# Kernel tuning notes

Hardware: AMD Instinct MI355X
Metric: run time of the kernel (lower is better)

## Reference

```python
import jax, jax.numpy as jnp
import numpy as np

B, S, D, K = 4, 4096, 1024, 64

def setup_inputs() -> dict:
    key = jax.random.key(0)
    kx, kq, kk, kv, ko = jax.random.split(key, 5)
    scale = 1.0 / np.sqrt(D)
    return {
        "x": jax.random.normal(kx, (B, S, D), dtype=jnp.float32),
        "Wq": jax.random.uniform(kq, (K, D), dtype=jnp.float32, minval=-scale, maxval=scale),
        "Wk": jax.random.uniform(kk, (K, D), dtype=jnp.float32, minval=-scale, maxval=scale),
        "Wv": jax.random.uniform(kv, (K, D), dtype=jnp.float32, minval=-scale, maxval=scale),
        "Wo": jax.random.uniform(ko, (D, K), dtype=jnp.float32, minval=-1.0/np.sqrt(K), maxval=1.0/np.sqrt(K)),
    }

def reference(x, Wq, Wk, Wv, Wo):
    # projections: torch Linear(dim, key_dim, bias=False) -> x @ W.T
    Q = jax.nn.elu(x @ Wq.T) + 1.0          # [B,S,K]
    Kf = jax.nn.elu(x @ Wk.T) + 1.0         # [B,S,K]
    V = x @ Wv.T                             # [B,S,K]
    # causal running KV state via cumsum of outer products: [B,S,K,K]
    KV_sum = jnp.cumsum(Kf[..., :, None] * V[..., None, :], axis=1)
    K_sum = jnp.cumsum(Kf, axis=1)           # [B,S,K]
    num = jnp.einsum('bsk,bskm->bsm', Q, KV_sum)   # [B,S,K]
    den = jnp.einsum('bsk,bsk->bs', Q, K_sum)[..., None]
    out = num / (den + 1e-6)
    return out @ Wo.T                         # [B,S,D]
```

## Files before the change

### kernel.cpp

```cpp
#include <hip/hip_runtime.h>

#define BB 4
#define SS 4096
#define DDIM 1024
#define KDIM 64
#define NCHUNK 64
#define TCHUNK 256
#define MROWS 16384

typedef short short8v __attribute__((ext_vector_type(8)));
typedef float f32x4 __attribute__((ext_vector_type(4)));
#define MFMA16 __builtin_amdgcn_mfma_f32_16x16x32_bf16

__device__ __forceinline__ ushort f2bf(float f) {
    uint u = __float_as_uint(f);
    u += 0x7FFFu + ((u >> 16) & 1u);
    return (ushort)(u >> 16);
}

__global__ __launch_bounds__(256) void k_wconv(
    const float* __restrict__ Wq, const float* __restrict__ Wk,
    const float* __restrict__ Wv, const float* __restrict__ Wo,
    ushort* __restrict__ Whf, ushort* __restrict__ Wof)
{
    const int b = blockIdx.x, t = threadIdx.x;
    const int ks = t >> 7;
    const int l = (t >> 1) & 63;
    const int half = t & 1;
    if (b < 192) {
        const int s = b / 12, cf = b % 12;
        const int grow = cf * 16 + (l & 15);
        const int gcol = s * 64 + ks * 32 + ((l >> 4) & 3) * 8 + half * 4;
        const float* src = (grow < 64) ? (Wq + (size_t)grow * DDIM)
                         : (grow < 128) ? (Wk + (size_t)(grow - 64) * DDIM)
                                        : (Wv + (size_t)(grow - 128) * DDIM);
        float4 v = *(const float4*)&src[gcol];
        ushort* dst = &Whf[(size_t)(((s * 12 + cf) * 2 + ks) * 64 + l) * 8 + half * 4];
        dst[0] = f2bf(v.x); dst[1] = f2bf(v.y); dst[2] = f2bf(v.z); dst[3] = f2bf(v.w);
    } else {
        const int cf = b - 192;
        const int d = cf * 16 + (l & 15);
        const int kc = ks * 32 + ((l >> 4) & 3) * 8 + half * 4;
        float4 v = *(const float4*)&Wo[(size_t)d * KDIM + kc];
        ushort* dst = &Wof[(size_t)((cf * 2 + ks) * 64 + l) * 8 + half * 4];
        dst[0] = f2bf(v.x); dst[1] = f2bf(v.y); dst[2] = f2bf(v.z); dst[3] = f2bf(v.w);
    }
}

#define EBP 216
__global__ __launch_bounds__(512) void k_proj(
    const float* __restrict__ x, const ushort* __restrict__ Whf,
    ushort* __restrict__ Qf, ushort* __restrict__ Kff, ushort* __restrict__ VT,
    float* __restrict__ KVc, float* __restrict__ Ksc)
{
    __shared__ ushort xs[2 * 64 * 512];
    const int t = threadIdx.x;
    const int w = t >> 6, l = t & 63;
    const int rw = w >> 2, cw = w & 3;
    const int g = blockIdx.x;
    const int row0 = g * 64;
    const int lq = l >> 4;

    float4 xr[16];
    auto stageLoad = [&](int h) {
#pragma unroll
        for (int i = 0; i < 8; ++i) {
            const int fidx = i * 512 + t;
            const int r = fidx >> 6;
            const int c = (fidx & 63) * 8;
            const float* p = &x[(size_t)(row0 + r) * DDIM + h * 512 + c];
            xr[i * 2] = *(const float4*)p;
            xr[i * 2 + 1] = *(const float4*)(p + 4);
        }
    };
    auto stageWrite = [&](int buf) {
        ushort* xb = xs + buf * 32768;
#pragma unroll
        for (int i = 0; i < 8; ++i) {
            const int fidx = i * 512 + t;
            const int r = fidx >> 6;
            const int c = (fidx & 63) * 8;
            float4 u0 = xr[i * 2], u1 = xr[i * 2 + 1];
            short8v hh;
            hh[0] = (short)f2bf(u0.x); hh[1] = (short)f2bf(u0.y);
            hh[2] = (short)f2bf(u0.z); hh[3] = (short)f2bf(u0.w);
            hh[4] = (short)f2bf(u1.x); hh[5] = (short)f2bf(u1.y);
            hh[6] = (short)f2bf(u1.z); hh[7] = (short)f2bf(u1.w);
            const int frag = (r >> 4) * 16 + (c >> 5);
            const int slot = ((r & 15) | (((c >> 3) & 3) << 4)) ^ (frag & 7);
            *(short8v*)&xb[(size_t)(frag * 64 + slot) * 8] = hh;
        }
    };

    f32x4 acc[2][3];
#pragma unroll
    for (int r = 0; r < 2; ++r)
#pragma unroll
        for (int c = 0; c < 3; ++c) acc[r][c] = (f32x4){0.f, 0.f, 0.f, 0.f};

    auto loadW = [&](int sg, short8v (&bw)[6]) {
#pragma unroll
        for (int j = 0; j < 6; ++j) {
            const int cf = cw * 3 + (j >> 1);
            const int f = cf * 2 + (j & 1);
            bw[j] = *(const short8v*)&Whf[((size_t)(sg * 24 + f)) * 512 + l * 8];
        }
    };
    auto computeStep = [&](int buf, int sl, short8v (&bw)[6]) {
        const ushort* xb = xs + buf * 32768;
#pragma unroll
        for (int ks = 0; ks < 2; ++ks) {
            const int kkl = sl * 2 + ks;
            const int f0 = (rw * 2) * 16 + kkl;
            const int f1 = (rw * 2 + 1) * 16 + kkl;
            short8v a0 = *(const short8v*)&xb[(size_t)(f0 * 64 + (l ^ (f0 & 7))) * 8];
            short8v a1 = *(const short8v*)&xb[(size_t)(f1 * 64 + (l ^ (f1 & 7))) * 8];
#pragma unroll
            for (int c = 0; c < 3; ++c) {
                acc[0][c] = MFMA16(a0, bw[c * 2 + ks], acc[0][c], 0, 0, 0);
                acc[1][c] = MFMA16(a1, bw[c * 2 + ks], acc[1][c], 0, 0, 0);
            }
        }
    };

    stageLoad(0); stageWrite(0);
    __syncthreads();
    stageLoad(1);
    {
        short8v bwA[6], bwB[6];
        loadW(0, bwA);
        for (int s = 0; s < 8; s += 2) {
            loadW(s + 1, bwB);
            computeStep(0, s, bwA);
            if (s + 2 < 8) loadW(s + 2, bwA);
            computeStep(0, s + 1, bwB);
        }
    }
    stageWrite(1);
    __syncthreads();
    {
        short8v bwA[6], bwB[6];
        loadW(8, bwA);
        for (int s = 0; s < 8; s += 2) {
            loadW(8 + s + 1, bwB);
            computeStep(1, s, bwA);
            if (s + 2 < 8) loadW(8 + s + 2, bwA);
            computeStep(1, s + 1, bwB);
        }
    }

    ushort* eb = xs;
#pragma unroll
    for (int rfi = 0; rfi < 2; ++rfi)
#pragma unroll
        for (int ci = 0; ci < 3; ++ci) {
            const int col = (cw * 3 + ci) * 16 + (l & 15);
#pragma unroll
            for (int q = 0; q < 4; ++q) {
                const int rl = (rw * 2 + rfi) * 16 + lq * 4 + q;
                float v = acc[rfi][ci][q];
                if (col < 128) v = (v > 0.f) ? v + 1.f : __expf(v);
                eb[rl * EBP + col] = f2bf(v);
            }
        }
    __syncthreads();

    {
        const int fj = t >> 6, lam = t & 63;
        const int rh = fj >> 2, rfm = (fj >> 1) & 1, ks = fj & 1;
        const int r = rh * 32 + rfm * 16 + (lam & 15);
        const int c0 = ks * 32 + ((lam >> 4) & 3) * 8;
        short8v q8 = *(const short8v*)&eb[r * EBP + c0];
        short8v k8 = *(const short8v*)&eb[r * EBP + 64 + c0];
        const size_t fo = ((size_t)((g * 2 + rh) * 4 + rfm * 2 + ks)) * 512 + lam * 8;
        *(short8v*)&Qf[fo] = q8;
        *(short8v*)&Kff[fo] = k8;
    }
    {
        const int fj = t >> 6, lam = t & 63;
        const int f = fj >> 1, js = fj & 1;
        const int jb = js * 32 + ((lam >> 4) & 3) * 8;
        const int vcol = 128 + f * 16 + (lam & 15);
        short8v vT;
#pragma unroll
        for (int e = 0; e < 8; ++e) vT[e] = (short)eb[(jb + e) * EBP + vcol];
        *(short8v*)&VT[((size_t)(g * 8 + f * 2 + js)) * 512 + lam * 8] = vT;
    }
    {
        const int kf = w & 3, mh = w >> 2;
        short8v ka[2], vb0[2], vb1[2];
#pragma unroll
        for (int js = 0; js < 2; ++js) {
            const int jb = js * 32 + ((l >> 4) & 3) * 8;
#pragma unroll
            for (int e = 0; e < 8; ++e) {
                const int j = jb + e;
                ka[js][e]  = (short)eb[j * EBP + 64 + kf * 16 + (l & 15)];
                vb0[js][e] = (short)eb[j * EBP + 128 + (mh * 2 + 0) * 16 + (l & 15)];
                vb1[js][e] = (short)eb[j * EBP + 128 + (mh * 2 + 1) * 16 + (l & 15)];
            }
        }
        f32x4 a0 = (f32x4){0.f,0.f,0.f,0.f}, a1 = (f32x4){0.f,0.f,0.f,0.f};
        f32x4 ad = (f32x4){0.f,0.f,0.f,0.f};
        short8v onesf;
#pragma unroll
        for (int e = 0; e < 8; ++e) onesf[e] = ((l & 15) == 0) ? (short)0x3F80 : (short)0;
#pragma unroll
        for (int js = 0; js < 2; ++js) {
            a0 = MFMA16(ka[js], vb0[js], a0, 0, 0, 0);
            a1 = MFMA16(ka[js], vb1[js], a1, 0, 0, 0);
            if (mh == 0) ad = MFMA16(ka[js], onesf, ad, 0, 0, 0);
        }
#pragma unroll
        for (int q = 0; q < 4; ++q) {
            const int k = kf * 16 + lq * 4 + q;
            KVc[(size_t)g * 4096 + k * 64 + (mh * 2 + 0) * 16 + (l & 15)] = a0[q];
            KVc[(size_t)g * 4096 + k * 64 + (mh * 2 + 1) * 16 + (l & 15)] = a1[q];
            if (mh == 0 && (l & 15) == 0) Ksc[(size_t)g * KDIM + k] = ad[q];
        }
    }
}

__global__ void k_scan(const float* __restrict__ KVc, const float* __restrict__ Ksc,
                       float* __restrict__ Sst, float* __restrict__ Kss)
{
    const int b = blockIdx.x / 65;
    const int r = blockIdx.x % 65;
    const int t = threadIdx.x;
    if (r < 64) {
        const int e = r * 64 + t;
        float v[64];
#pragma unroll
        for (int i = 0; i < 64; ++i)
            v[i] = KVc[((size_t)(b * NCHUNK + i)) * 4096 + e];
        float acc = 0.f;
#pragma unroll
        for (int i = 0; i < 64; ++i) {
            Sst[((size_t)(b * NCHUNK + i)) * 4096 + e] = acc;
            acc += v[i];
        }
    } else {
        float v[64];
#pragma unroll
        for (int i = 0; i < 64; ++i)
            v[i] = Ksc[((size_t)(b * NCHUNK + i)) * KDIM + t];
        float acc = 0.f;
#pragma unroll
        for (int i = 0; i < 64; ++i) {
            Kss[((size_t)(b * NCHUNK + i)) * KDIM + t] = acc;
            acc += v[i];
        }
    }
}

__global__ __launch_bounds__(256) void k_intra(
    const ushort* __restrict__ Qf, const ushort* __restrict__ Kff,
    const ushort* __restrict__ VT, const float* __restrict__ Sst,
    const float* __restrict__ Kss, const ushort* __restrict__ Wof,
    float* __restrict__ out)
{
    __shared__ ushort pb[32 * 64];
    __shared__ ushort sT[80 * 64];
    __shared__ float ob[4][16 * 68 + 4];
    const int bx = blockIdx.x, t = threadIdx.x;
    const int g = bx >> 1, rh = bx & 1;
    const int w = t >> 6, l = t & 63;
    const int lq = l >> 4;

    {
        const int k = t >> 2, m0 = (t & 3) * 16;
        const float4* sp = (const float4*)&Sst[(size_t)g * 4096 + k * 64 + m0];
        float4 f0 = sp[0], f1 = sp[1], f2v = sp[2], f3 = sp[3];
        float fv[16] = {f0.x, f0.y, f0.z, f0.w, f1.x, f1.y, f1.z, f1.w,
                        f2v.x, f2v.y, f2v.z, f2v.w, f3.x, f3.y, f3.z, f3.w};
#pragma unroll
        for (int i = 0; i < 16; ++i) {
            const int m = m0 + i;
            sT[m * 64 + (k ^ ((m & 7) << 3))] = f2bf(fv[i]);
        }
        if (t < 64) sT[64 * 64 + t] = f2bf(Kss[(size_t)g * KDIM + t]);
        for (int idx = t; idx < 960; idx += 256) sT[65 * 64 + idx] = 0;
    }

    const int rf = w & 1;
    short8v qa[2];
#pragma unroll
    for (int ks = 0; ks < 2; ++ks)
        qa[ks] = *(const short8v*)&Qf[((size_t)((g * 2 + rh) * 4 + rf * 2 + ks)) * 512 + l * 8];
    {
        const int cfh = w >> 1;
        f32x4 accs[2];
#pragma unroll
        for (int ci = 0; ci < 2; ++ci) accs[ci] = (f32x4){0.f, 0.f, 0.f, 0.f};
#pragma unroll
        for (int ci = 0; ci < 2; ++ci) {
            const int cf = cfh * 2 + ci;
#pragma unroll
            for (int ks = 0; ks < 2; ++ks) {
                short8v kb = *(const short8v*)&Kff[((size_t)((g * 2 + (cf >> 1)) * 4 + (cf & 1) * 2 + ks)) * 512 + l * 8];
                accs[ci] = MFMA16(qa[ks], kb, accs[ci], 0, 0, 0);
            }
        }
#pragma unroll
        for (int ci = 0; ci < 2; ++ci)
#pragma unroll
            for (int q = 0; q < 4; ++q) {
                const int row = rf * 16 + lq * 4 + q;
                const int col = (cfh * 2 + ci) * 16 + (l & 15);
                const float sv = (col <= rh * 32 + row) ? accs[ci][q] : 0.f;
                pb[row * 64 + (col ^ ((row & 7) << 3))] = f2bf(sv);
            }
    }
    __syncthreads();

    const int mg = w >> 1;
    f32x4 an0 = (f32x4){0.f,0.f,0.f,0.f}, an1 = (f32x4){0.f,0.f,0.f,0.f};
    f32x4 ad = (f32x4){0.f,0.f,0.f,0.f};
    short8v onesf;
#pragma unroll
    for (int e = 0; e < 8; ++e) onesf[e] = ((l & 15) == 0) ? (short)0x3F80 : (short)0;
#pragma unroll
    for (int js = 0; js < 2; ++js) {
        const int prow = rf * 16 + (l & 15);
        const int pbase = js * 32 + ((l >> 4) & 3) * 8;
        short8v pa = *(const short8v*)&pb[prow * 64 + (pbase ^ ((prow & 7) << 3))];
        short8v v0 = *(const short8v*)&VT[((size_t)(g * 8 + (mg * 2 + 0) * 2 + js)) * 512 + l * 8];
        short8v v1 = *(const short8v*)&VT[((size_t)(g * 8 + (mg * 2 + 1) * 2 + js)) * 512 + l * 8];
        an0 = MFMA16(pa, v0, an0, 0, 0, 0);
        an1 = MFMA16(pa, v1, an1, 0, 0, 0);
        ad  = MFMA16(pa, onesf, ad, 0, 0, 0);
    }
#pragma unroll
    for (int ks = 0; ks < 2; ++ks) {
        const int base = ks * 32 + ((l >> 4) & 3) * 8;
        const int r0 = (mg * 2 + 0) * 16 + (l & 15);
        const int r1 = (mg * 2 + 1) * 16 + (l & 15);
        const int r4 = 64 + (l & 15);
        short8v s0 = *(const short8v*)&sT[r0 * 64 + (base ^ ((r0 & 7) << 3))];
        short8v s1 = *(const short8v*)&sT[r1 * 64 + (base ^ ((r1 & 7) << 3))];
        short8v s4 = *(const short8v*)&sT[r4 * 64 + (base ^ ((r4 & 7) << 3))];
        an0 = MFMA16(qa[ks], s0, an0, 0, 0, 0);
        an1 = MFMA16(qa[ks], s1, an1, 0, 0, 0);
        ad  = MFMA16(qa[ks], s4, ad, 0, 0, 0);
    }
#pragma unroll
    for (int q = 0; q < 4; ++q) {
        const float den = __shfl(ad[q], (l & 48));
        const float rinv = 1.f / (den + 1e-6f);
        const int row = rf * 16 + lq * 4 + q;
        const int c0 = (mg * 2 + 0) * 16 + (l & 15);
        const int c1 = (mg * 2 + 1) * 16 + (l & 15);
        pb[row * 64 + (c0 ^ ((row & 7) << 3))] = f2bf(an0[q] * rinv);
        pb[row * 64 + (c1 ^ ((row & 7) << 3))] = f2bf(an1[q] * rinv);
    }
    __syncthreads();

    short8v oa[2][2];
#pragma unroll
    for (int rfi = 0; rfi < 2; ++rfi)
#pragma unroll
        for (int ks = 0; ks < 2; ++ks) {
            const int row = rfi * 16 + (l & 15);
            const int base = ks * 32 + ((l >> 4) & 3) * 8;
            oa[rfi][ks] = *(const short8v*)&pb[row * 64 + (base ^ ((row & 7) << 3))];
        }
    float* obw = ob[w];
#pragma unroll
    for (int rr = 0; rr < 4; ++rr) {
        f32x4 acco[2][4];
#pragma unroll
        for (int rfi = 0; rfi < 2; ++rfi)
#pragma unroll
            for (int ci = 0; ci < 4; ++ci) acco[rfi][ci] = (f32x4){0.f, 0.f, 0.f, 0.f};
#pragma unroll
        for (int ci = 0; ci < 4; ++ci) {
            const int cfg = w * 16 + rr * 4 + ci;
#pragma unroll
            for (int ks = 0; ks < 2; ++ks) {
                short8v wb = *(const short8v*)&Wof[((size_t)(cfg * 2 + ks)) * 512 + l * 8];
#pragma unroll
                for (int rfi = 0; rfi < 2; ++rfi)
                    acco[rfi][ci] = MFMA16(oa[rfi][ks], wb, acco[rfi][ci], 0, 0, 0);
            }
        }
#pragma unroll
        for (int rfi = 0; rfi < 2; ++rfi) {
#pragma unroll
            for (int ci = 0; ci < 4; ++ci)
#pragma unroll
                for (int q = 0; q < 4; ++q)
                    obw[(lq * 4 + q) * 68 + ci * 16 + (l & 15)] = acco[rfi][ci][q];
#pragma unroll
            for (int rg = 0; rg < 4; ++rg) {
                const int row = rg * 4 + lq;
                float4 vv = *(const float4*)&obw[row * 68 + (l & 15) * 4];
                *(float4*)&out[((size_t)(g * 64 + rh * 32 + rfi * 16 + row)) * DDIM
                               + w * 256 + rr * 64 + (l & 15) * 4] = vv;
            }
        }
    }
}

extern "C" void kernel_launch(void* const* d_in, const int* in_sizes, int n_in,
                              void* d_out, int out_size, void* d_ws, size_t ws_size,
                              hipStream_t stream)
{
    const float* x  = (const float*)d_in[0];
    const float* Wq = (const float*)d_in[1];
    const float* Wk = (const float*)d_in[2];
    const float* Wv = (const float*)d_in[3];
    const float* Wo = (const float*)d_in[4];
    float* out = (float*)d_out;

    float* ws   = (float*)d_ws;
    float* KVc  = ws;
    float* Sst  = KVc + (size_t)TCHUNK * 4096;
    float* Ksc  = Sst + (size_t)TCHUNK * 4096;
    float* Kss  = Ksc + (size_t)TCHUNK * KDIM;
    ushort* Whf = (ushort*)(Kss + (size_t)TCHUNK * KDIM);
    ushort* Wof = Whf + (size_t)192 * DDIM;
    ushort* Qf  = Wof + (size_t)64 * 1024;
    ushort* Kff = Qf  + (size_t)512 * 4 * 512;
    ushort* VT  = Kff + (size_t)512 * 4 * 512;

    k_wconv<<<dim3(256), dim3(256), 0, stream>>>(Wq, Wk, Wv, Wo, Whf, Wof);
    k_proj<<<dim3(TCHUNK), dim3(512), 0, stream>>>(x, Whf, Qf, Kff, VT, KVc, Ksc);
    k_scan<<<dim3(BB * 65), dim3(64), 0, stream>>>(KVc, Ksc, Sst, Kss);
    k_intra<<<dim3(TCHUNK * 2), dim3(256), 0, stream>>>(Qf, Kff, VT, Sst, Kss, Wof, out);
}
```

Measured before the change: 56.80 us.

## Halve projection tile to 32 rows and split chunk KV sums into new kernel

New measurement: 57.97 us. 1.02x slower.

```diff
diff --git a/kernel.cpp b/kernel.cpp
--- a/kernel.cpp
+++ b/kernel.cpp
@@ -50,53 +50,41 @@
 #define EBP 216
 __global__ __launch_bounds__(512) void k_proj(
     const float* __restrict__ x, const ushort* __restrict__ Whf,
-    ushort* __restrict__ Qf, ushort* __restrict__ Kff, ushort* __restrict__ VT,
-    float* __restrict__ KVc, float* __restrict__ Ksc)
-{
-    __shared__ ushort xs[2 * 64 * 512];
+    ushort* __restrict__ Qf, ushort* __restrict__ Kff,
+    ushort* __restrict__ KfT, ushort* __restrict__ VT)
+{
+    __shared__ ushort xs[64 * 512];
     const int t = threadIdx.x;
     const int w = t >> 6, l = t & 63;
     const int rw = w >> 2, cw = w & 3;
-    const int g = blockIdx.x;
-    const int row0 = g * 64;
+    const int mb = blockIdx.x;
+    const int row0 = mb * 32;
     const int lq = l >> 4;
 
-    float4 xr[16];
-    auto stageLoad = [&](int h) {
+    {
 #pragma unroll
         for (int i = 0; i < 8; ++i) {
-            const int fidx = i * 512 + t;
-            const int r = fidx >> 6;
-            const int c = (fidx & 63) * 8;
-            const float* p = &x[(size_t)(row0 + r) * DDIM + h * 512 + c];
-            xr[i * 2] = *(const float4*)p;
-            xr[i * 2 + 1] = *(const float4*)(p + 4);
-        }
-    };
-    auto stageWrite = [&](int buf) {
-        ushort* xb = xs + buf * 32768;
-#pragma unroll
-        for (int i = 0; i < 8; ++i) {
-            const int fidx = i * 512 + t;
-            const int r = fidx >> 6;
-            const int c = (fidx & 63) * 8;
-            float4 u0 = xr[i * 2], u1 = xr[i * 2 + 1];
+            const int c8 = i * 512 + t;
+            const int r = c8 >> 7;
+            const int col = (c8 & 127) * 8;
+            const float* p = &x[(size_t)(row0 + r) * DDIM + col];
+            float4 u0 = *(const float4*)p;
+            float4 u1 = *(const float4*)(p + 4);
             short8v hh;
             hh[0] = (short)f2bf(u0.x); hh[1] = (short)f2bf(u0.y);
             hh[2] = (short)f2bf(u0.z); hh[3] = (short)f2bf(u0.w);
             hh[4] = (short)f2bf(u1.x); hh[5] = (short)f2bf(u1.y);
             hh[6] = (short)f2bf(u1.z); hh[7] = (short)f2bf(u1.w);
-            const int frag = (r >> 4) * 16 + (c >> 5);
-            const int slot = ((r & 15) | (((c >> 3) & 3) << 4)) ^ (frag & 7);
-            *(short8v*)&xb[(size_t)(frag * 64 + slot) * 8] = hh;
-        }
-    };
-
-    f32x4 acc[2][3];
-#pragma unroll
-    for (int r = 0; r < 2; ++r)
-#pragma unroll
-        for (int c = 0; c < 3; ++c) acc[r][c] = (f32x4){0.f, 0.f, 0.f, 0.f};
+            const int frag = (r >> 4) * 32 + (col >> 5);
+            const int slot = ((r & 15) | (((col >> 3) & 3) << 4)) ^ (frag & 7);
+            *(short8v*)&xs[(size_t)(frag * 64 + slot) * 8] = hh;
+        }
+    }
+    __syncthreads();
+
+    f32x4 acc[3];
+#pragma unroll
+    for (int c = 0; c < 3; ++c) acc[c] = (f32x4){0.f, 0.f, 0.f, 0.f};
 
     auto loadW = [&](int sg, short8v (&bw)[6]) {
 #pragma unroll
@@ -106,117 +94,113 @@
             bw[j] = *(const short8v*)&Whf[((size_t)(sg * 24 + f)) * 512 + l * 8];
         }
     };
-    auto computeStep = [&](int buf, int sl, short8v (&bw)[6]) {
-        const ushort* xb = xs + buf * 32768;
+    auto computeStep = [&](int sl, short8v (&bw)[6]) {
 #pragma unroll
         for (int ks = 0; ks < 2; ++ks) {
-            const int kkl = sl * 2 + ks;
-            const int f0 = (rw * 2) * 16 + kkl;
-            const int f1 = (rw * 2 + 1) * 16 + kkl;
-            short8v a0 = *(const short8v*)&xb[(size_t)(f0 * 64 + (l ^ (f0 & 7))) * 8];
-            short8v a1 = *(const short8v*)&xb[(size_t)(f1 * 64 + (l ^ (f1 & 7))) * 8];
-#pragma unroll
-            for (int c = 0; c < 3; ++c) {
-                acc[0][c] = MFMA16(a0, bw[c * 2 + ks], acc[0][c], 0, 0, 0);
-                acc[1][c] = MFMA16(a1, bw[c * 2 + ks], acc[1][c], 0, 0, 0);
-            }
+            const int f = rw * 32 + sl * 2 + ks;
+            short8v a = *(const short8v*)&xs[(size_t)(f * 64 + (l ^ (f & 7))) * 8];
+#pragma unroll
+            for (int c = 0; c < 3; ++c)
+                acc[c] = MFMA16(a, bw[c * 2 + ks], acc[c], 0, 0, 0);
         }
     };
 
-    stageLoad(0); stageWrite(0);
-    __syncthreads();
-    stageLoad(1);
     {
         short8v bwA[6], bwB[6];
         loadW(0, bwA);
-        for (int s = 0; s < 8; s += 2) {
+        for (int s = 0; s < 16; s += 2) {
             loadW(s + 1, bwB);
-            computeStep(0, s, bwA);
-            if (s + 2 < 8) loadW(s + 2, bwA);
-            computeStep(0, s + 1, bwB);
-        }
-    }
-    stageWrite(1);
+            computeStep(s, bwA);
+            if (s + 2 < 16) loadW(s + 2, bwA);
+            computeStep(s + 1, bwB);
+        }
+    }
+
     __syncthreads();
-    {
-        short8v bwA[6], bwB[6];
-        loadW(8, bwA);
-        for (int s = 0; s < 8; s += 2) {
-            loadW(8 + s + 1, bwB);
-            computeStep(1, s, bwA);
-            if (s + 2 < 8) loadW(8 + s + 2, bwA);
-            computeStep(1, s + 1, bwB);
-        }
-    }
-
     ushort* eb = xs;
 #pragma unroll
-    for (int rfi = 0; rfi < 2; ++rfi)
-#pragma unroll
-        for (int ci = 0; ci < 3; ++ci) {
-            const int col = (cw * 3 + ci) * 16 + (l & 15);
-#pragma unroll
-            for (int q = 0; q < 4; ++q) {
-                const int rl = (rw * 2 + rfi) * 16 + lq * 4 + q;
-                float v = acc[rfi][ci][q];
-                if (col < 128) v = (v > 0.f) ? v + 1.f : __expf(v);
-                eb[rl * EBP + col] = f2bf(v);
-            }
-        }
+    for (int ci = 0; ci < 3; ++ci) {
+        const int col = (cw * 3 + ci) * 16 + (l & 15);
+#pragma unroll
+        for (int q = 0; q < 4; ++q) {
+            const int row = rw * 16 + lq * 4 + q;
+            float v = acc[ci][q];
+            if (col < 128) v = (v > 0.f) ? v + 1.f : __expf(v);
+            eb[row * EBP + col] = f2bf(v);
+        }
+    }
     __syncthreads();
 
     {
-        const int fj = t >> 6, lam = t & 63;
-        const int rh = fj >> 2, rfm = (fj >> 1) & 1, ks = fj & 1;
-        const int r = rh * 32 + rfm * 16 + (lam & 15);
-        const int c0 = ks * 32 + ((lam >> 4) & 3) * 8;
-        short8v q8 = *(const short8v*)&eb[r * EBP + c0];
-        short8v k8 = *(const short8v*)&eb[r * EBP + 64 + c0];
-        const size_t fo = ((size_t)((g * 2 + rh) * 4 + rfm * 2 + ks)) * 512 + lam * 8;
-        *(short8v*)&Qf[fo] = q8;
-        *(short8v*)&Kff[fo] = k8;
-    }
-    {
-        const int fj = t >> 6, lam = t & 63;
-        const int f = fj >> 1, js = fj & 1;
-        const int jb = js * 32 + ((lam >> 4) & 3) * 8;
-        const int vcol = 128 + f * 16 + (lam & 15);
-        short8v vT;
-#pragma unroll
-        for (int e = 0; e < 8; ++e) vT[e] = (short)eb[(jb + e) * EBP + vcol];
-        *(short8v*)&VT[((size_t)(g * 8 + f * 2 + js)) * 512 + lam * 8] = vT;
-    }
-    {
-        const int kf = w & 3, mh = w >> 2;
-        short8v ka[2], vb0[2], vb1[2];
+        const int fj = t >> 6;
+        const int which = fj >> 2, rf = (fj >> 1) & 1, ks = fj & 1;
+        const int r = rf * 16 + (l & 15);
+        const int c0 = ks * 32 + ((l >> 4) & 3) * 8;
+        const size_t fo = ((size_t)(mb * 4 + rf * 2 + ks)) * 512 + l * 8;
+        if (which == 0) {
+            short8v q8 = *(const short8v*)&eb[r * EBP + c0];
+            *(short8v*)&Qf[fo] = q8;
+        } else {
+            short8v k8 = *(const short8v*)&eb[r * EBP + 64 + c0];
+            *(short8v*)&Kff[fo] = k8;
+        }
+    }
+    {
+        const int fj = t >> 6;
+        const int which = fj >> 2, f = fj & 3;
+        const int col = (which ? 128 : 64) + f * 16 + (l & 15);
+        const int jb = ((l >> 4) & 3) * 8;
+        short8v tv;
+#pragma unroll
+        for (int e = 0; e < 8; ++e) tv[e] = (short)eb[(jb + e) * EBP + col];
+        const size_t fo = ((size_t)((mb >> 1) * 8 + f * 2 + (mb & 1))) * 512 + l * 8;
+        if (which == 0) *(short8v*)&KfT[fo] = tv;
+        else            *(short8v*)&VT[fo]  = tv;
+    }
+}
+
+__global__ __launch_bounds__(64) void k_chunksum(
+    const ushort* __restrict__ KfT, const ushort* __restrict__ VT,
+    float* __restrict__ KVc, float* __restrict__ Ksc)
+{
+    const int g = blockIdx.x, l = threadIdx.x;
+    short8v ka[4][2], vb[4][2];
+#pragma unroll
+    for (int f = 0; f < 4; ++f)
 #pragma unroll
         for (int js = 0; js < 2; ++js) {
-            const int jb = js * 32 + ((l >> 4) & 3) * 8;
-#pragma unroll
-            for (int e = 0; e < 8; ++e) {
-                const int j = jb + e;
-                ka[js][e]  = (short)eb[j * EBP + 64 + kf * 16 + (l & 15)];
-                vb0[js][e] = (short)eb[j * EBP + 128 + (mh * 2 + 0) * 16 + (l & 15)];
-                vb1[js][e] = (short)eb[j * EBP + 128 + (mh * 2 + 1) * 16 + (l & 15)];
-            }
-        }
-        f32x4 a0 = (f32x4){0.f,0.f,0.f,0.f}, a1 = (f32x4){0.f,0.f,0.f,0.f};
-        f32x4 ad = (f32x4){0.f,0.f,0.f,0.f};
-        short8v onesf;
-#pragma unroll
-        for (int e = 0; e < 8; ++e) onesf[e] = ((l & 15) == 0) ? (short)0x3F80 : (short)0;
-#pragma unroll
-        for (int js = 0; js < 2; ++js) {
-            a0 = MFMA16(ka[js], vb0[js], a0, 0, 0, 0);
-            a1 = MFMA16(ka[js], vb1[js], a1, 0, 0, 0);
-            if (mh == 0) ad = MFMA16(ka[js], onesf, ad, 0, 0, 0);
-        }
+            const size_t fo = ((size_t)(g * 8 + f * 2 + js)) * 512 + l * 8;
+            ka[f][js] = *(const short8v*)&KfT[fo];
+            vb[f][js] = *(const short8v*)&VT[fo];
+        }
+    short8v onesf;
+#pragma unroll
+    for (int e = 0; e < 8; ++e) onesf[e] = ((l & 15) == 0) ? (short)0x3F80 : (short)0;
+
+    f32x4 acc[4][5];
+#pragma unroll
+    for (int kf = 0; kf < 4; ++kf)
+#pragma unroll
+        for (int mf = 0; mf < 5; ++mf) acc[kf][mf] = (f32x4){0.f, 0.f, 0.f, 0.f};
+#pragma unroll
+    for (int js = 0; js < 2; ++js)
+#pragma unroll
+        for (int kf = 0; kf < 4; ++kf) {
+#pragma unroll
+            for (int mf = 0; mf < 4; ++mf)
+                acc[kf][mf] = MFMA16(ka[kf][js], vb[mf][js], acc[kf][mf], 0, 0, 0);
+            acc[kf][4] = MFMA16(ka[kf][js], onesf, acc[kf][4], 0, 0, 0);
+        }
+    const int lq = l >> 4;
+#pragma unroll
+    for (int kf = 0; kf < 4; ++kf) {
 #pragma unroll
         for (int q = 0; q < 4; ++q) {
             const int k = kf * 16 + lq * 4 + q;
-            KVc[(size_t)g * 4096 + k * 64 + (mh * 2 + 0) * 16 + (l & 15)] = a0[q];
-            KVc[(size_t)g * 4096 + k * 64 + (mh * 2 + 1) * 16 + (l & 15)] = a1[q];
-            if (mh == 0 && (l & 15) == 0) Ksc[(size_t)g * KDIM + k] = ad[q];
+#pragma unroll
+            for (int mf = 0; mf < 4; ++mf)
+                KVc[(size_t)g * 4096 + k * 64 + mf * 16 + (l & 15)] = acc[kf][mf][q];
+            if ((l & 15) == 0) Ksc[(size_t)g * KDIM + k] = acc[kf][4][q];
         }
     }
 }
@@ -421,10 +405,12 @@
     ushort* Wof = Whf + (size_t)192 * DDIM;
     ushort* Qf  = Wof + (size_t)64 * 1024;
     ushort* Kff = Qf  + (size_t)512 * 4 * 512;
-    ushort* VT  = Kff + (size_t)512 * 4 * 512;
+    ushort* KfT = Kff + (size_t)512 * 4 * 512;
+    ushort* VT  = KfT + (size_t)256 * 8 * 512;
 
     k_wconv<<<dim3(256), dim3(256), 0, stream>>>(Wq, Wk, Wv, Wo, Whf, Wof);
-    k_proj<<<dim3(TCHUNK), dim3(512), 0, stream>>>(x, Whf, Qf, Kff, VT, KVc, Ksc);
+    k_proj<<<dim3(MROWS / 32), dim3(512), 0, stream>>>(x, Whf, Qf, Kff, KfT, VT);
+    k_chunksum<<<dim3(TCHUNK), dim3(64), 0, stream>>>(KfT, VT, KVc, Ksc);
     k_scan<<<dim3(BB * 65), dim3(64), 0, stream>>>(KVc, Ksc, Sst, Kss);
     k_intra<<<dim3(TCHUNK * 2), dim3(256), 0, stream>>>(Qf, Kff, VT, Sst, Kss, Wof, out);
 }
```
